# Performance work log

Hardware: AMD Instinct MI355X
Metric: run time of the kernel (lower is better)

The kernel has to match this reference:

```python
import jax, jax.numpy as jnp
import numpy as np

D = 16
EPS = 1e-15


def setup_inputs() -> dict:
    key = jax.random.key(0)
    k1, k2 = jax.random.split(key)
    B, C, H, W = 8, 384, 64, 64  # C = heads(8) * 3 * D(16)
    K = 512
    qkv = jax.random.normal(k1, (B, C, H, W), dtype=jnp.float32)
    codebook = jax.random.normal(k2, (K, D), dtype=jnp.float32)
    return {"qkv": qkv, "codebook": codebook}


def reference(qkv, codebook):
    B, C, H, W = qkv.shape
    K = codebook.shape[0]
    # (B, heads, 3D, HW) -> (B, heads, HW, 3D)
    x = qkv.reshape(B, -1, 3 * D, H * W).transpose(0, 1, 3, 2)
    q = x[..., 0:D].reshape(-1, D)          # (N, D)
    k = x[..., D:2 * D].reshape(-1, D)      # (N, D)
    v = x[..., 2 * D:].reshape(-1, D)       # (N, D)
    # vector quantization: nearest codebook entry by squared L2
    # ||k - c||^2 = ||k||^2 - 2 k.c + ||c||^2 ; ||k||^2 constant over argmin
    dist = jnp.sum(codebook * codebook, axis=-1)[None, :] - 2.0 * (k @ codebook.T)
    indices = jnp.argmin(dist, axis=-1)     # (N,) int, detached (non-diff)
    # O_tV = one_hot.T @ v  -> per-code sum of v
    O_tV = jax.ops.segment_sum(v, indices, num_segments=K)          # (K, D)
    # counts = one_hot.T @ ones  (denominator collapses to exp(QC_t) @ counts)
    counts = jax.ops.segment_sum(jnp.ones_like(indices, dtype=q.dtype), indices, num_segments=K)  # (K,)
    QC_t = q @ codebook.T                   # (N, K)
    E = jnp.exp(QC_t)                       # (N, K)
    numerator = E @ O_tV                    # (N, D)
    denominator = E @ counts + EPS          # (N,)
    result = numerator / denominator[:, None]
    return result.reshape(B, -1, H, W)      # (B, heads*D, H, W)
```

## Files before the change

### kernel.cpp

```cpp
#include <hip/hip_runtime.h>

typedef short short8 __attribute__((ext_vector_type(8)));
typedef float floatx4 __attribute__((ext_vector_type(4)));

#define D16 16
#define KC 512
#define NTOK (8 * 8 * 4096)


__device__ __forceinline__ unsigned short rne_bf16(float x) {
    unsigned u = __float_as_uint(x);
    return (unsigned short)((u + 0x7fffu + ((u >> 16) & 1u)) >> 16);
}
__device__ __forceinline__ float bf16_to_f32(unsigned short h) {
    return __uint_as_float(((unsigned)h) << 16);
}

extern "C" __global__ __launch_bounds__(256)
void vq_assign(const float* __restrict__ qkv, const float* __restrict__ cb,
               unsigned short* __restrict__ idx)
{
    __shared__ alignas(16) unsigned short s_cbh[KC * 16];
    __shared__ alignas(16) unsigned short s_cbr[KC * 16];
    __shared__ float s_cn[KC];
    __shared__ float s_kf[4][16][17];
    int tid = threadIdx.x;
    for (int i = tid; i < KC * 16; i += 256) {
        float x = cb[i];
        unsigned short h = rne_bf16(x);
        s_cbh[i] = h;
        s_cbr[i] = rne_bf16(x - bf16_to_f32(h));
    }
    for (int j = tid; j < KC; j += 256) {
        float s = 0.f;
#pragma unroll
        for (int d = 0; d < D16; ++d) { float c = cb[j * D16 + d]; s = fmaf(c, c, s); }
        s_cn[j] = s;
    }
    __syncthreads();

    int lane = tid & 63;
    int col = lane & 15;
    int half8 = ((lane >> 4) & 1) * 8;
    bool hiHalf = lane < 32;
    int wv = tid >> 6;
    int tile0 = (blockIdx.x * 4 + wv) * 4;

    for (int t = 0; t < 4; ++t) {
        int tok0 = (tile0 + t) * 16;
        int bh = tok0 >> 12;
        const float* kbase = qkv + (size_t)bh * (48 * 4096) + 16 * 4096 + (tok0 & 4095);

        short8 a8;
        {
            const float* p = kbase + (size_t)half8 * 4096 + col;
#pragma unroll
            for (int i = 0; i < 8; ++i) {
                float x = p[(size_t)i * 4096];
                unsigned short h = rne_bf16(x);
                a8[i] = hiHalf ? (short)h : (short)rne_bf16(x - bf16_to_f32(h));
                if (hiHalf) s_kf[wv][col][half8 + i] = x;
            }
        }
        __builtin_amdgcn_wave_barrier();

        float p1[4], p2[4];
#pragma unroll
        for (int r = 0; r < 4; ++r) { p1[r] = -3.4e38f; p2[r] = -3.4e38f; }

        for (int c = 0; c < 32; ++c) {
            int code = c * 16 + col;
            short8 b1 = *(const short8*)(&s_cbh[code * 16 + half8]);
            short8 b2 = (short8)0;
            if (hiHalf) b2 = *(const short8*)(&s_cbr[code * 16 + half8]);
            float cn2 = -0.5f * s_cn[code];
            floatx4 acc = { cn2, cn2, cn2, cn2 };
            acc = __builtin_amdgcn_mfma_f32_16x16x32_bf16(a8, b1, acc, 0, 0, 0);
            acc = __builtin_amdgcn_mfma_f32_16x16x32_bf16(a8, b2, acc, 0, 0, 0);
#pragma unroll
            for (int r = 0; r < 4; ++r) {
                unsigned sb = (__float_as_uint(acc[r]) & 0xFFFFFE00u) | (unsigned)code;
                float sp = __uint_as_float(sb);
                float old1 = p1[r];
                p1[r] = fmaxf(old1, sp);
                p2[r] = fmaxf(p2[r], fminf(old1, sp));
            }
        }
#pragma unroll
        for (int m = 1; m < 16; m <<= 1) {
#pragma unroll
            for (int r = 0; r < 4; ++r) {
                float o1 = __shfl_xor(p1[r], m, 64);
                float o2 = __shfl_xor(p2[r], m, 64);
                float n1 = fmaxf(p1[r], o1);
                float n2 = fmaxf(fminf(p1[r], o1), fmaxf(p2[r], o2));
                p1[r] = n1; p2[r] = n2;
            }
        }
        if (col < 4) {
            int c1 = 0, c2 = 0;
#pragma unroll
            for (int r = 0; r < 4; ++r) {
                if (col == r) {
                    c1 = (int)(__float_as_uint(p1[r]) & 511u);
                    c2 = (int)(__float_as_uint(p2[r]) & 511u);
                }
            }
            int tokrow = (lane >> 4) * 4 + col;
            const float* kf = &s_kf[wv][tokrow][0];
            const float* cb1 = cb + c1 * D16;
            const float* cb2 = cb + c2 * D16;
            float dot1 = 0.f, dot2 = 0.f;
#pragma unroll
            for (int d = 0; d < D16; ++d) {
                float kx = kf[d];
                dot1 = fmaf(kx, cb1[d], dot1);
                dot2 = fmaf(kx, cb2[d], dot2);
            }
            float d1 = fmaf(-2.f, dot1, s_cn[c1]);
            float d2 = fmaf(-2.f, dot2, s_cn[c2]);
            int jw = (d2 < d1 || (d2 == d1 && c2 < c1)) ? c2 : c1;
            idx[tok0 + tokrow] = (unsigned short)jw;
        }
        __builtin_amdgcn_wave_barrier();
    }
}

extern "C" __global__ __launch_bounds__(256)
void vq_segsum(const float* __restrict__ qkv, const unsigned short* __restrict__ idx,
               float* __restrict__ M)
{
    __shared__ float s_acc[KC * 17];
    for (int i = threadIdx.x; i < KC * 17; i += 256) s_acc[i] = 0.f;
    __syncthreads();

    for (int n = blockIdx.x * 256 + threadIdx.x; n < NTOK; n += gridDim.x * 256) {
        int bh = n >> 12, hw = n & 4095;
        const float* bv = qkv + (size_t)bh * (48 * 4096) + hw + 32 * 4096;
        int bj = idx[n];
#pragma unroll
        for (int d = 0; d < D16; ++d)
            atomicAdd(&s_acc[bj * 17 + d], bv[d * 4096]);
        atomicAdd(&s_acc[bj * 17 + 16], 1.0f);
    }
    __syncthreads();
    for (int i = threadIdx.x; i < KC * 17; i += 256)
        atomicAdd(&M[i], s_acc[i]);
}

extern "C" __global__ __launch_bounds__(256)
void vq_attend(const float* __restrict__ qkv, const float* __restrict__ cb,
               const float* __restrict__ M, float* __restrict__ out)
{
    __shared__ alignas(16) unsigned short s_cbh[KC * 16];
    __shared__ alignas(16) unsigned short s_cbr[KC * 16];
    __shared__ alignas(16) unsigned short s_mt[16 * 520];
    __shared__ float s_cnt[KC];
    __shared__ alignas(16) unsigned short s_wh[4][16 * 40];
    __shared__ alignas(16) unsigned short s_wr[4][16 * 40];

    int tid = threadIdx.x;
    for (int i = tid; i < KC * 16; i += 256) {
        float x = cb[i];
        unsigned short h = rne_bf16(x);
        s_cbh[i] = h;
        s_cbr[i] = rne_bf16(x - bf16_to_f32(h));
    }
    for (int i = tid; i < KC * 17; i += 256) {
        int j = i / 17, d = i - j * 17;
        float x = M[i];
        if (d == 16) s_cnt[j] = x;
        else s_mt[d * 520 + j] = rne_bf16(x);
    }
    __syncthreads();

    int lane = tid & 63;
    int col = lane & 15;
    int half8 = ((lane >> 4) & 1) * 8;
    bool hiHalf = lane < 32;
    int wv_id = tid >> 6;
    unsigned short* wlh = &s_wh[wv_id][0];
    unsigned short* wlr = &s_wr[wv_id][0];
    int tile0 = (blockIdx.x * 4 + wv_id) * 4;

    for (int t = 0; t < 4; ++t) {
        int tok0 = (tile0 + t) * 16;
        int bh = tok0 >> 12;
        const float* qbase = qkv + (size_t)bh * (48 * 4096) + (tok0 & 4095);

        short8 a8;
        {
            const float* p = qbase + (size_t)half8 * 4096 + col;
#pragma unroll
            for (int i = 0; i < 8; ++i) {
                float x = p[(size_t)i * 4096];
                unsigned short h = rne_bf16(x);
                a8[i] = hiHalf ? (short)h : (short)rne_bf16(x - bf16_to_f32(h));
            }
        }

        floatx4 oacc = {0.f, 0.f, 0.f, 0.f};
        float den[4] = {0.f, 0.f, 0.f, 0.f};

        for (int c = 0; c < 32; ++c) {
            int code = c * 16 + col;
            short8 b1 = *(const short8*)(&s_cbh[code * 16 + half8]);
            short8 b2 = (short8)0;
            if (hiHalf) b2 = *(const short8*)(&s_cbr[code * 16 + half8]);
            floatx4 s = {0.f, 0.f, 0.f, 0.f};
            s = __builtin_amdgcn_mfma_f32_16x16x32_bf16(a8, b1, s, 0, 0, 0);
            s = __builtin_amdgcn_mfma_f32_16x16x32_bf16(a8, b2, s, 0, 0, 0);

            float cnt = s_cnt[code];
            int cl = (c & 1) * 16 + col;
#pragma unroll
            for (int r = 0; r < 4; ++r) {
                float wv = __expf(s[r]);
                unsigned short wbh = rne_bf16(wv);
                unsigned short wbr = rne_bf16(wv - bf16_to_f32(wbh));
                den[r] = fmaf(wv, cnt, den[r]);
                int widx = ((lane >> 4) * 4 + r) * 40 + cl;
                wlh[widx] = wbh;
                wlr[widx] = wbr;
            }
            if (c & 1) {
                int aoff = (lane & 15) * 40 + (lane >> 4) * 8;
                short8 wah = *(const short8*)(&wlh[aoff]);
                short8 war = *(const short8*)(&wlr[aoff]);
                short8 mb = *(const short8*)(&s_mt[(lane & 15) * 520 + (c - 1) * 16 + (lane >> 4) * 8]);
                oacc = __builtin_amdgcn_mfma_f32_16x16x32_bf16(wah, mb, oacc, 0, 0, 0);
                oacc = __builtin_amdgcn_mfma_f32_16x16x32_bf16(war, mb, oacc, 0, 0, 0);
            }
        }
#pragma unroll
        for (int m = 1; m < 16; m <<= 1) {
#pragma unroll
            for (int r = 0; r < 4; ++r) den[r] += __shfl_xor(den[r], m, 64);
        }
#pragma unroll
        for (int r = 0; r < 4; ++r) {
            int row = (lane >> 4) * 4 + r;
            float o = oacc[r] / (den[r] + 1e-15f);
            out[(size_t)(tok0 + row) * D16 + col] = o;
        }
    }
}

extern "C" void kernel_launch(void* const* d_in, const int* in_sizes, int n_in,
                              void* d_out, int out_size, void* d_ws, size_t ws_size,
                              hipStream_t stream) {
    const float* qkv = (const float*)d_in[0];
    const float* cb  = (const float*)d_in[1];
    float* out = (float*)d_out;

    float* M = (float*)d_ws;
    unsigned short* idx = (unsigned short*)((char*)d_ws + 36864);

    hipMemsetAsync(d_ws, 0, KC * 17 * sizeof(float), stream);

    vq_assign<<<NTOK / 256, 256, 0, stream>>>(qkv, cb, idx);
    vq_segsum<<<256, 256, 0, stream>>>(qkv, idx, M);
    vq_attend<<<NTOK / 256, 256, 0, stream>>>(qkv, cb, M, out);
}
```

Baseline: 280.7 us.

## Process two token tiles per wave and restructure exp-weight MFMA layout

The attend kernel now handles two 16-token tiles at once per wave, sharing codebook fragment loads between two interleaved MFMA chains. The exp weights are split into hi/residual parts with truncation instead of RNE and written to a swizzled LDS tile holding hi and residual side by side, so one MFMA per code chunk per tile covers K=32 in a single step instead of two MFMAs every other iteration. This cuts LDS loads and rounding instructions and adds independent MFMA work to hide latency. The costs are higher register pressure and slightly different numerics from truncating the split.

After: 256.7 us. -8.6%, faster.

```diff
diff --git a/kernel.cpp b/kernel.cpp
--- a/kernel.cpp
+++ b/kernel.cpp
@@ -156,8 +156,7 @@
     __shared__ alignas(16) unsigned short s_cbr[KC * 16];
     __shared__ alignas(16) unsigned short s_mt[16 * 520];
     __shared__ float s_cnt[KC];
-    __shared__ alignas(16) unsigned short s_wh[4][16 * 40];
-    __shared__ alignas(16) unsigned short s_wr[4][16 * 40];
+    __shared__ alignas(16) unsigned short s_w[4][2][16 * 40];
 
     int tid = threadIdx.x;
     for (int i = tid; i < KC * 16; i += 256) {
@@ -176,72 +175,96 @@
 
     int lane = tid & 63;
     int col = lane & 15;
-    int half8 = ((lane >> 4) & 1) * 8;
+    int g = lane >> 4;
+    int half8 = (g & 1) * 8;
     bool hiHalf = lane < 32;
     int wv_id = tid >> 6;
-    unsigned short* wlh = &s_wh[wv_id][0];
-    unsigned short* wlr = &s_wr[wv_id][0];
+    unsigned short* wtA = &s_w[wv_id][0][0];
+    unsigned short* wtB = &s_w[wv_id][1][0];
     int tile0 = (blockIdx.x * 4 + wv_id) * 4;
 
-    for (int t = 0; t < 4; ++t) {
-        int tok0 = (tile0 + t) * 16;
-        int bh = tok0 >> 12;
-        const float* qbase = qkv + (size_t)bh * (48 * 4096) + (tok0 & 4095);
-
-        short8 a8;
+    int wr_row = g * 4;
+    int w_wr_hi = ((col >> 3) ^ g) << 3;
+    int w_wr_re = (((col >> 3) + 2) ^ g) << 3;
+    int w_rd = col * 40 + ((g ^ (col >> 2)) << 3);
+
+    for (int tp = 0; tp < 2; ++tp) {
+        int tokA = (tile0 + 2 * tp) * 16;
+        int tokB = tokA + 16;
+
+        short8 aA, aB;
         {
-            const float* p = qbase + (size_t)half8 * 4096 + col;
+            const float* p = qkv + (size_t)(tokA >> 12) * (48 * 4096) + (tokA & 4095)
+                           + (size_t)half8 * 4096 + col;
 #pragma unroll
             for (int i = 0; i < 8; ++i) {
                 float x = p[(size_t)i * 4096];
                 unsigned short h = rne_bf16(x);
-                a8[i] = hiHalf ? (short)h : (short)rne_bf16(x - bf16_to_f32(h));
-            }
-        }
-
-        floatx4 oacc = {0.f, 0.f, 0.f, 0.f};
-        float den[4] = {0.f, 0.f, 0.f, 0.f};
+                aA[i] = hiHalf ? (short)h : (short)rne_bf16(x - bf16_to_f32(h));
+            }
+        }
+        {
+            const float* p = qkv + (size_t)(tokB >> 12) * (48 * 4096) + (tokB & 4095)
+                           + (size_t)half8 * 4096 + col;
+#pragma unroll
+            for (int i = 0; i < 8; ++i) {
+                float x = p[(size_t)i * 4096];
+                unsigned short h = rne_bf16(x);
+                aB[i] = hiHalf ? (short)h : (short)rne_bf16(x - bf16_to_f32(h));
+            }
+        }
+
+        floatx4 oA = {0.f, 0.f, 0.f, 0.f}, oB = {0.f, 0.f, 0.f, 0.f};
+        float denA[4] = {0.f, 0.f, 0.f, 0.f}, denB[4] = {0.f, 0.f, 0.f, 0.f};
 
         for (int c = 0; c < 32; ++c) {
             int code = c * 16 + col;
             short8 b1 = *(const short8*)(&s_cbh[code * 16 + half8]);
             short8 b2 = (short8)0;
             if (hiHalf) b2 = *(const short8*)(&s_cbr[code * 16 + half8]);
-            floatx4 s = {0.f, 0.f, 0.f, 0.f};
-            s = __builtin_amdgcn_mfma_f32_16x16x32_bf16(a8, b1, s, 0, 0, 0);
-            s = __builtin_amdgcn_mfma_f32_16x16x32_bf16(a8, b2, s, 0, 0, 0);
+
+            floatx4 sA = {0.f, 0.f, 0.f, 0.f}, sB = {0.f, 0.f, 0.f, 0.f};
+            sA = __builtin_amdgcn_mfma_f32_16x16x32_bf16(aA, b1, sA, 0, 0, 0);
+            sB = __builtin_amdgcn_mfma_f32_16x16x32_bf16(aB, b1, sB, 0, 0, 0);
+            sA = __builtin_amdgcn_mfma_f32_16x16x32_bf16(aA, b2, sA, 0, 0, 0);
+            sB = __builtin_amdgcn_mfma_f32_16x16x32_bf16(aB, b2, sB, 0, 0, 0);
 
             float cnt = s_cnt[code];
-            int cl = (c & 1) * 16 + col;
-#pragma unroll
-            for (int r = 0; r < 4; ++r) {
-                float wv = __expf(s[r]);
-                unsigned short wbh = rne_bf16(wv);
-                unsigned short wbr = rne_bf16(wv - bf16_to_f32(wbh));
-                den[r] = fmaf(wv, cnt, den[r]);
-                int widx = ((lane >> 4) * 4 + r) * 40 + cl;
-                wlh[widx] = wbh;
-                wlr[widx] = wbr;
-            }
-            if (c & 1) {
-                int aoff = (lane & 15) * 40 + (lane >> 4) * 8;
-                short8 wah = *(const short8*)(&wlh[aoff]);
-                short8 war = *(const short8*)(&wlr[aoff]);
-                short8 mb = *(const short8*)(&s_mt[(lane & 15) * 520 + (c - 1) * 16 + (lane >> 4) * 8]);
-                oacc = __builtin_amdgcn_mfma_f32_16x16x32_bf16(wah, mb, oacc, 0, 0, 0);
-                oacc = __builtin_amdgcn_mfma_f32_16x16x32_bf16(war, mb, oacc, 0, 0, 0);
-            }
+#pragma unroll
+            for (int r = 0; r < 4; ++r) {
+                int base = (wr_row + r) * 40 + (col & 7);
+                float wA = __expf(sA[r]);
+                unsigned uA = __float_as_uint(wA);
+                float rsA = wA - __uint_as_float(uA & 0xffff0000u);
+                denA[r] = fmaf(wA, cnt, denA[r]);
+                wtA[base + w_wr_hi] = (unsigned short)(uA >> 16);
+                wtA[base + w_wr_re] = (unsigned short)(__float_as_uint(rsA) >> 16);
+                float wB = __expf(sB[r]);
+                unsigned uB = __float_as_uint(wB);
+                float rsB = wB - __uint_as_float(uB & 0xffff0000u);
+                denB[r] = fmaf(wB, cnt, denB[r]);
+                wtB[base + w_wr_hi] = (unsigned short)(uB >> 16);
+                wtB[base + w_wr_re] = (unsigned short)(__float_as_uint(rsB) >> 16);
+            }
+            short8 mb = *(const short8*)(&s_mt[col * 520 + c * 16 + half8]);
+            short8 wfA = *(const short8*)(&wtA[w_rd]);
+            short8 wfB = *(const short8*)(&wtB[w_rd]);
+            oA = __builtin_amdgcn_mfma_f32_16x16x32_bf16(wfA, mb, oA, 0, 0, 0);
+            oB = __builtin_amdgcn_mfma_f32_16x16x32_bf16(wfB, mb, oB, 0, 0, 0);
         }
 #pragma unroll
         for (int m = 1; m < 16; m <<= 1) {
 #pragma unroll
-            for (int r = 0; r < 4; ++r) den[r] += __shfl_xor(den[r], m, 64);
+            for (int r = 0; r < 4; ++r) {
+                denA[r] += __shfl_xor(denA[r], m, 64);
+                denB[r] += __shfl_xor(denB[r], m, 64);
+            }
         }
 #pragma unroll
         for (int r = 0; r < 4; ++r) {
-            int row = (lane >> 4) * 4 + r;
-            float o = oacc[r] / (den[r] + 1e-15f);
-            out[(size_t)(tok0 + row) * D16 + col] = o;
+            int row = g * 4 + r;
+            out[(size_t)(tokA + row) * D16 + col] = oA[r] / (denA[r] + 1e-15f);
+            out[(size_t)(tokB + row) * D16 + col] = oB[r] / (denB[r] + 1e-15f);
         }
     }
 }
```
